# Kernel tuning notes

Measured on AMD Instinct MI355X. Metric: run time of the kernel, lower is better.

The kernel has to match this reference:

```python
import jax, jax.numpy as jnp
import numpy as np

N_NODES = 100000
N_EDGES = 1000000
D_FEAT = 64
N_GRAPHS = 64


def setup_inputs() -> dict:
    key = jax.random.key(0)
    ks = jax.random.split(key, 5)
    x = jax.random.normal(ks[0], (N_NODES, D_FEAT), dtype=jnp.float32)
    edge_index = jax.random.randint(ks[1], (2, N_EDGES), 0, N_NODES, dtype=jnp.int32)
    batch = jnp.sort(jax.random.randint(ks[2], (N_NODES,), 0, N_GRAPHS, dtype=jnp.int32))
    s = 1.0 / np.sqrt(D_FEAT)
    W1 = jax.random.uniform(ks[3], (D_FEAT, D_FEAT), jnp.float32, -s, s)
    W2 = jax.random.uniform(ks[4], (D_FEAT, D_FEAT), jnp.float32, -s, s)
    b1 = jnp.zeros((D_FEAT,), jnp.float32)
    b2 = jnp.zeros((D_FEAT,), jnp.float32)
    return {"x": x, "edge_index": edge_index, "batch": batch,
            "W1": W1, "b1": b1, "W2": W2, "b2": b2}


def gcn_conv(x, edge_index, W, b, num_nodes):
    # PyG GCNConv: h = D^{-1/2} (A + I) D^{-1/2} (x W) + b
    loops = jnp.arange(num_nodes, dtype=edge_index.dtype)
    row = jnp.concatenate([edge_index[0], loops])  # source nodes
    col = jnp.concatenate([edge_index[1], loops])  # target nodes
    h = x @ W  # [N, D]
    deg = jax.ops.segment_sum(jnp.ones_like(col, dtype=h.dtype), col,
                              num_segments=num_nodes)  # >= 1 due to self loops
    dinv = jax.lax.rsqrt(deg)
    norm = dinv[row] * dinv[col]  # [E+N]
    out = jax.ops.segment_sum(h[row] * norm[:, None], col, num_segments=num_nodes)
    return out + b


def reference(x, edge_index, batch, W1, b1, W2, b2):
    n = x.shape[0]
    h = gcn_conv(x, edge_index, W1, b1, n)
    h = gcn_conv(h, edge_index, W2, b2, n)
    # global_mean_pool over graph ids
    sums = jax.ops.segment_sum(h, batch, num_segments=N_GRAPHS)  # [G, D]
    cnts = jax.ops.segment_sum(jnp.ones((n, 1), h.dtype), batch,
                               num_segments=N_GRAPHS)
    return sums / jnp.maximum(cnts, 1.0)
```

## Files before the change

kernel.cpp:

```cpp
#include <hip/hip_runtime.h>
#include <hip/hip_fp16.h>

#define DFEAT 64
#define NG 64
#define TILE 128
#define NBLK 256
#define NBMAX 1024
#define NREP 16
#define SENT 0x7FFFFFFF

__global__ __launch_bounds__(256) void k_cnt(const int* __restrict__ col,
                                             int* __restrict__ cnt_m,
                                             int e, int nb, int chunk) {
  __shared__ int hist[NBMAX];
  int tid = threadIdx.x;
  int blk = blockIdx.x;
  for (int b = tid; b < nb; b += 256) hist[b] = 0;
  __syncthreads();
  int lo = blk * chunk, hi = min(lo + chunk, e);
  if (lo < hi) {
    int nv = (hi - lo) >> 2;
    const int4* c4 = (const int4*)(col + lo);
    for (int i = tid; i < nv; i += 256) {
      int4 v = c4[i];
      atomicAdd(&hist[v.x >> 7], 1);
      atomicAdd(&hist[v.y >> 7], 1);
      atomicAdd(&hist[v.z >> 7], 1);
      atomicAdd(&hist[v.w >> 7], 1);
    }
    for (int i = lo + (nv << 2) + tid; i < hi; i += 256)
      atomicAdd(&hist[col[i] >> 7], 1);
  }
  __syncthreads();
  for (int b = tid; b < nb; b += 256)
    cnt_m[(size_t)blk * nb + b] = hist[b];
}

__global__ __launch_bounds__(256) void k_colscan(int* __restrict__ cnt_m,
                                                 int* __restrict__ gcount, int nb) {
  __shared__ int sh[256];
  int tid = threadIdx.x;
  int b = blockIdx.x;
  int v = cnt_m[(size_t)tid * nb + b];
  sh[tid] = v;
  __syncthreads();
  for (int off = 1; off < 256; off <<= 1) {
    int t = (tid >= off) ? sh[tid - off] : 0;
    __syncthreads();
    sh[tid] += t;
    __syncthreads();
  }
  cnt_m[(size_t)tid * nb + b] = sh[tid] - v;
  if (tid == 255) gcount[b] = sh[255];
}

__global__ __launch_bounds__(1024) void k_bscan(const int* __restrict__ gcount,
                                                int* __restrict__ base, int nb,
                                                const float* __restrict__ W1,
                                                const float* __restrict__ W2,
                                                const float* __restrict__ b1,
                                                const int* __restrict__ batch,
                                                float* __restrict__ WW,
                                                float* __restrict__ bw,
                                                float* __restrict__ cntf, int n) {
  __shared__ float shm[8192];
  int tid = threadIdx.x;
  if (blockIdx.x == 0) {
    int* sh = (int*)shm;
    int v = (tid < nb) ? gcount[tid] : 0;
    sh[tid] = v;
    __syncthreads();
    for (int off = 1; off < 1024; off <<= 1) {
      int t = (tid >= off) ? sh[tid - off] : 0;
      __syncthreads();
      sh[tid] += t;
      __syncthreads();
    }
    if (tid < nb) base[tid] = sh[tid] - v;
    if (tid == 0) base[nb] = sh[1023];
  } else {
    float* w1 = shm;
    float* w2 = shm + 4096;
    for (int i = tid; i < 4096; i += 1024) { w1[i] = W1[i]; w2[i] = W2[i]; }
    if (tid < NG) {
      int g = tid;
      int lo = 0, hi = n;
      while (lo < hi) { int m = (lo + hi) >> 1; if (batch[m] < g) lo = m + 1; else hi = m; }
      int a = lo;
      lo = 0; hi = n;
      while (lo < hi) { int m = (lo + hi) >> 1; if (batch[m] < g + 1) lo = m + 1; else hi = m; }
      cntf[g] = (float)(lo - a);
    }
    __syncthreads();
    for (int p = tid; p < 4096; p += 1024) {
      int k = p >> 6, d = p & 63;
      float a = 0.f;
      for (int m = 0; m < 64; ++m) a += w1[k * 64 + m] * w2[m * 64 + d];
      WW[p] = a;
    }
    if (tid < 64) {
      float a = 0.f;
      for (int k = 0; k < 64; ++k) a += b1[k] * w2[k * 64 + tid];
      bw[tid] = a;
    }
  }
}

__global__ __launch_bounds__(256) void k_bin2(const int* __restrict__ row,
                                              const int* __restrict__ col,
                                              const int* __restrict__ base,
                                              const int* __restrict__ cnt_m,
                                              int* __restrict__ pairs,
                                              int e, int nb, int chunk) {
  __shared__ int gl[NBMAX];
  __shared__ int lcur[NBMAX];
  int tid = threadIdx.x;
  int blk = blockIdx.x;
  for (int b = tid; b < nb; b += 256) {
    gl[b] = base[b] + cnt_m[(size_t)blk * nb + b];
    lcur[b] = 0;
  }
  __syncthreads();
  int lo = blk * chunk, hi = min(lo + chunk, e);
  if (lo >= hi) return;
  int nv = (hi - lo) >> 2;
  const int4* r4 = (const int4*)(row + lo);
  const int4* c4 = (const int4*)(col + lo);
  for (int i = tid; i < nv; i += 256) {
    int4 rs = r4[i];
    int4 ts = c4[i];
#pragma unroll
    for (int k = 0; k < 4; ++k) {
      int s = (&rs.x)[k], t = (&ts.x)[k];
      int b = t >> 7;
      int pos = gl[b] + atomicAdd(&lcur[b], 1);
      pairs[pos] = s | ((t & (TILE - 1)) << 20);
    }
  }
  for (int i = lo + (nv << 2) + tid; i < hi; i += 256) {
    int s = row[i], t = col[i];
    int b = t >> 7;
    int pos = gl[b] + atomicAdd(&lcur[b], 1);
    pairs[pos] = s | ((t & (TILE - 1)) << 20);
  }
}

__global__ __launch_bounds__(256) void k_csr(const int* __restrict__ pairs,
                                             const int* __restrict__ base,
                                             const float* __restrict__ x,
                                             int* __restrict__ starts,
                                             int* __restrict__ srcs,
                                             float* __restrict__ dinv,
                                             __half2* __restrict__ xh,
                                             int* __restrict__ order,
                                             int n, int e) {
  __shared__ int cnt[TILE];
  __shared__ int cur[TILE];
  __shared__ int sc[TILE];
  __shared__ float sdv[TILE];
  __shared__ int dh[64], dcur[64];
  int tid = threadIdx.x;
  int b = blockIdx.x;
  int tile0 = b * TILE;
  if (tid < TILE) cnt[tid] = 0;
  if (tid >= TILE && tid < TILE + 64) dh[tid - TILE] = 0;
  __syncthreads();
  int e0 = base[b], e1 = base[b + 1];
  for (int i = e0 + tid; i < e1; i += 256)
    atomicAdd(&cnt[(unsigned)pairs[i] >> 20], 1);
  __syncthreads();
  int c = (tid < TILE) ? cnt[tid] : 0;
  if (tid < TILE) sc[tid] = c;
  __syncthreads();
  for (int off = 1; off < TILE; off <<= 1) {
    int t = (tid < TILE && tid >= off) ? sc[tid - off] : 0;
    __syncthreads();
    if (tid < TILE) sc[tid] += t;
    __syncthreads();
  }
  int mybin = 63;
  if (tid < TILE) {
    int excl = sc[tid] - c;
    cur[tid] = excl;
    int node = tile0 + tid;
    float d = rsqrtf(1.0f + (float)c);
    sdv[tid] = (node < n) ? d : 0.f;
    if (node < n) {
      starts[node] = e0 + excl;
      dinv[node] = d;
      mybin = min(c, 62);
    }
    atomicAdd(&dh[mybin], 1);
  }
  if (b == 0 && tid == 0) starts[n] = e;
  __syncthreads();
  if (tid == 0) {
    int a = 0;
    for (int i = 0; i < 64; ++i) { int t = dh[i]; dcur[i] = a; a += t; }
  }
  __syncthreads();
  if (tid < TILE) {
    int rank = atomicAdd(&dcur[mybin], 1);
    int node = tile0 + tid;
    order[tile0 + rank] = (node < n) ? node : SENT;
  }
  for (int i = e0 + tid; i < e1; i += 256) {
    int p = pairs[i];
    int pos = atomicAdd(&cur[(unsigned)p >> 20], 1);
    srcs[e0 + pos] = p & 0xFFFFF;
  }
  int nnode = min(n - tile0, TILE);
  if (nnode > 0) {
    int nfl = nnode * 16;
    const float4* xf = (const float4*)(x + (size_t)tile0 * 64);
    float2* xo = (float2*)xh + (size_t)tile0 * 16;
    for (int p = tid; p < nfl; p += 256) {
      float4 v = xf[p];
      float d = sdv[p >> 4];
      float2 st;
      ((__half2*)&st)[0] = __floats2half2_rn(v.x * d, v.y * d);
      ((__half2*)&st)[1] = __floats2half2_rn(v.z * d, v.w * d);
      xo[p] = st;
    }
  }
}

__device__ __forceinline__ void acc8w(float2& a0, float2& a1, float2& a2,
                                      float2& a3, float4 v, float w) {
  const __half2* hp = (const __half2*)&v;
  float2 t;
  t = __half22float2(hp[0]); a0.x = fmaf(w, t.x, a0.x); a0.y = fmaf(w, t.y, a0.y);
  t = __half22float2(hp[1]); a1.x = fmaf(w, t.x, a1.x); a1.y = fmaf(w, t.y, a1.y);
  t = __half22float2(hp[2]); a2.x = fmaf(w, t.x, a2.x); a2.y = fmaf(w, t.y, a2.y);
  t = __half22float2(hp[3]); a3.x = fmaf(w, t.x, a3.x); a3.y = fmaf(w, t.y, a3.y);
}
__device__ __forceinline__ void acc8(float2& a0, float2& a1, float2& a2,
                                     float2& a3, float4 v) {
  const __half2* hp = (const __half2*)&v;
  float2 t;
  t = __half22float2(hp[0]); a0.x += t.x; a0.y += t.y;
  t = __half22float2(hp[1]); a1.x += t.x; a1.y += t.y;
  t = __half22float2(hp[2]); a2.x += t.x; a2.y += t.y;
  t = __half22float2(hp[3]); a3.x += t.x; a3.y += t.y;
}

__global__ __launch_bounds__(256) void k_gather1(const int* __restrict__ starts,
                                                 const int* __restrict__ srcs,
                                                 const float* __restrict__ dinv,
                                                 const __half2* __restrict__ xh,
                                                 const int* __restrict__ batch,
                                                 const int* __restrict__ order,
                                                 __half2* __restrict__ z1h,
                                                 float* __restrict__ Tr, int n) {
  int tid = threadIdx.x;
  int slot = blockIdx.x * 32 + (tid >> 3);
  int node = order[slot];
  bool act = node < n;
  int nc = act ? node : n - 1;
  int l = tid & 7;
  int lane = tid & 63;
  int rep = blockIdx.x & (NREP - 1);
  int s = starts[nc];
  int deg = act ? (starts[nc + 1] - s) : 0;
  float dc = dinv[nc];
  int g = batch[nc];
  const float4* xf = (const float4*)xh;
  float4 sv = xf[(size_t)nc * 8 + l];
  float2 a0 = make_float2(0.f, 0.f), a1 = a0, a2 = a0, a3 = a0;
  acc8(a0, a1, a2, a3, sv);
  float wsum = 0.f;
  int trips = (deg + 3) >> 2;
  int dm1 = deg - 1;
  int r0 = 0, r1 = 0, r2 = 0, r3 = 0;
  if (trips > 0) {
    r0 = srcs[s];
    r1 = srcs[s + min(1, dm1)];
    r2 = srcs[s + min(2, dm1)];
    r3 = srcs[s + min(3, dm1)];
  }
  int j = 0;
  for (int t = 0; t < trips; ++t) {
    int n0 = r0, n1 = r1, n2 = r2, n3 = r3;
    int jn = j + 4;
    r0 = srcs[s + min(jn + 0, dm1)];
    r1 = srcs[s + min(jn + 1, dm1)];
    r2 = srcs[s + min(jn + 2, dm1)];
    r3 = srcs[s + min(jn + 3, dm1)];
    float w1w = (j + 1 < deg) ? 1.f : 0.f;
    float w2w = (j + 2 < deg) ? 1.f : 0.f;
    float w3w = (j + 3 < deg) ? 1.f : 0.f;
    float4 v0 = xf[(size_t)n0 * 8 + l];
    float4 v1 = xf[(size_t)n1 * 8 + l];
    float4 v2 = xf[(size_t)n2 * 8 + l];
    float4 v3 = xf[(size_t)n3 * 8 + l];
    wsum += dinv[n0] + w1w * dinv[n1] + w2w * dinv[n2] + w3w * dinv[n3];
    acc8(a0, a1, a2, a3, v0);
    acc8w(a0, a1, a2, a3, v1, w1w);
    acc8w(a0, a1, a2, a3, v2, w2w);
    acc8w(a0, a1, a2, a3, v3, w3w);
    j = jn;
  }
  if (act) {
    float s2 = dc * dc;
    float4 ov;
    __half2* op = (__half2*)&ov;
    op[0] = __floats2half2_rn(s2 * a0.x, s2 * a0.y);
    op[1] = __floats2half2_rn(s2 * a1.x, s2 * a1.y);
    op[2] = __floats2half2_rn(s2 * a2.x, s2 * a2.y);
    op[3] = __floats2half2_rn(s2 * a3.x, s2 * a3.y);
    ((float4*)z1h)[(size_t)node * 8 + l] = ov;
  }
  float uval = act ? dc * (dc + wsum) : 0.f;
  int g0 = __shfl(g, 0);
  bool uni = (__all(g == g0) != 0);
  if (!uni) {
    if (act && l == 0) unsafeAtomicAdd(&Tr[rep * NG + g], uval);
  } else {
    float uv = (l == 0) ? uval : 0.f;
    uv += __shfl_xor(uv, 8);
    uv += __shfl_xor(uv, 16);
    uv += __shfl_xor(uv, 32);
    if (lane == 0 && uv != 0.f) unsafeAtomicAdd(&Tr[rep * NG + g0], uv);
  }
}

__global__ __launch_bounds__(256) void k_gather2(const int* __restrict__ starts,
                                                 const int* __restrict__ srcs,
                                                 const float* __restrict__ dinv,
                                                 const __half2* __restrict__ z1h,
                                                 const int* __restrict__ batch,
                                                 const int* __restrict__ order,
                                                 float* __restrict__ Pb,
                                                 float* __restrict__ S, int n) {
  __shared__ float rowacc[2][64];
  __shared__ int sgid[2];
  int tid = threadIdx.x;
  int blk0 = (int)blockIdx.x * 32;
  int slot = blk0 + (tid >> 3);
  int node = order[slot];
  bool act = node < n;
  int nc = act ? node : n - 1;
  int l = tid & 7;
  int lane = tid & 63;
  int s = starts[nc];
  int deg = act ? (starts[nc + 1] - s) : 0;
  float dc = dinv[nc];
  int g = batch[nc];
  if (tid < 128) ((float*)rowacc)[tid] = 0.f;
  if (tid < 2) {
    int tile0b = blk0 & ~(TILE - 1);
    int idx = tile0b + (tid ? (TILE - 1) : 0);
    if (idx > n - 1) idx = n - 1;
    sgid[tid] = batch[idx];
  }
  const float4* xf = (const float4*)z1h;
  float4 sv = xf[(size_t)nc * 8 + l];
  float2 a0 = make_float2(0.f, 0.f), a1 = a0, a2 = a0, a3 = a0;
  acc8(a0, a1, a2, a3, sv);
  int trips = (deg + 3) >> 2;
  int dm1 = deg - 1;
  int r0 = 0, r1 = 0, r2 = 0, r3 = 0;
  if (trips > 0) {
    r0 = srcs[s];
    r1 = srcs[s + min(1, dm1)];
    r2 = srcs[s + min(2, dm1)];
    r3 = srcs[s + min(3, dm1)];
  }
  int j = 0;
  for (int t = 0; t < trips; ++t) {
    int n0 = r0, n1 = r1, n2 = r2, n3 = r3;
    int jn = j + 4;
    r0 = srcs[s + min(jn + 0, dm1)];
    r1 = srcs[s + min(jn + 1, dm1)];
    r2 = srcs[s + min(jn + 2, dm1)];
    r3 = srcs[s + min(jn + 3, dm1)];
    float w1w = (j + 1 < deg) ? 1.f : 0.f;
    float w2w = (j + 2 < deg) ? 1.f : 0.f;
    float w3w = (j + 3 < deg) ? 1.f : 0.f;
    float4 v0 = xf[(size_t)n0 * 8 + l];
    float4 v1 = xf[(size_t)n1 * 8 + l];
    float4 v2 = xf[(size_t)n2 * 8 + l];
    float4 v3 = xf[(size_t)n3 * 8 + l];
    acc8(a0, a1, a2, a3, v0);
    acc8w(a0, a1, a2, a3, v1, w1w);
    acc8w(a0, a1, a2, a3, v2, w2w);
    acc8w(a0, a1, a2, a3, v3, w3w);
    j = jn;
  }
  float f[8];
  f[0] = act ? dc * a0.x : 0.f;
  f[1] = act ? dc * a0.y : 0.f;
  f[2] = act ? dc * a1.x : 0.f;
  f[3] = act ? dc * a1.y : 0.f;
  f[4] = act ? dc * a2.x : 0.f;
  f[5] = act ? dc * a2.y : 0.f;
  f[6] = act ? dc * a3.x : 0.f;
  f[7] = act ? dc * a3.y : 0.f;
  __syncthreads();
  int g_lo = sgid[0], g_hi = sgid[1];
  int sel = (g == g_lo) ? 0 : ((g == g_hi) ? 1 : -1);
  if (sel < 0 && act) {
#pragma unroll
    for (int k = 0; k < 8; ++k)
      unsafeAtomicAdd(&S[g * 64 + l * 8 + k], f[k]);
  }
  float fa[8], fb[8];
#pragma unroll
  for (int k = 0; k < 8; ++k) {
    fa[k] = (sel == 0) ? f[k] : 0.f;
    fb[k] = (sel == 1) ? f[k] : 0.f;
  }
#pragma unroll
  for (int k = 0; k < 8; ++k) {
    fa[k] += __shfl_xor(fa[k], 8);
    fa[k] += __shfl_xor(fa[k], 16);
    fa[k] += __shfl_xor(fa[k], 32);
    fb[k] += __shfl_xor(fb[k], 8);
    fb[k] += __shfl_xor(fb[k], 16);
    fb[k] += __shfl_xor(fb[k], 32);
  }
  if (lane < 8) {
#pragma unroll
    for (int k = 0; k < 8; ++k) {
      if (fa[k] != 0.f) atomicAdd(&rowacc[0][lane * 8 + k], fa[k]);
      if (fb[k] != 0.f) atomicAdd(&rowacc[1][lane * 8 + k], fb[k]);
    }
  }
  __syncthreads();
  float* pb = Pb + (size_t)blockIdx.x * 130;
  if (tid < 128) pb[tid] = ((float*)rowacc)[tid];
  if (tid == 128) pb[128] = (float)g_lo;
  if (tid == 129) pb[129] = (float)g_hi;
}

__global__ __launch_bounds__(256) void k_fin(const float* __restrict__ Pb,
                                             const int* __restrict__ batch,
                                             const float* __restrict__ S,
                                             const float* __restrict__ Tr,
                                             const float* __restrict__ cntf,
                                             const float* __restrict__ WW,
                                             const float* __restrict__ bw,
                                             const float* __restrict__ b2,
                                             float* __restrict__ out, int n,
                                             int nbw) {
  __shared__ float sh[4][64];
  __shared__ float sG[64];
  int g = blockIdx.x;
  int d = threadIdx.x & 63, r = threadIdx.x >> 6;
  int lo = 0, hi = n;
  while (lo < hi) { int m = (lo + hi) >> 1; if (batch[m] < g) lo = m + 1; else hi = m; }
  int a = lo;
  lo = 0; hi = n;
  while (lo < hi) { int m = (lo + hi) >> 1; if (batch[m] < g + 1) lo = m + 1; else hi = m; }
  int b = lo;
  float acc = 0.f;
  if (b > a) {
    int bl0 = (a >> 7) << 2;
    int bl1 = min((((b - 1) >> 7) << 2) + 3, nbw - 1);
    for (int bl = bl0 + r; bl <= bl1; bl += 4) {
      const float* p = Pb + (size_t)bl * 130;
      if ((int)p[128] == g) acc += p[d];
      if ((int)p[129] == g) acc += p[64 + d];
    }
  }
  sh[r][d] = acc;
  __syncthreads();
  if (r == 0) sG[d] = acc + sh[1][d] + sh[2][d] + sh[3][d] + S[g * 64 + d];
  __syncthreads();
  if (threadIdx.x < 64) {
    float aa = 0.f;
    for (int k = 0; k < 64; ++k) aa += sG[k] * WW[k * 64 + d];
    float T = 0.f;
    for (int rr = 0; rr < NREP; ++rr) T += Tr[rr * NG + g];
    float c = fmaxf(cntf[g], 1.0f);
    out[g * 64 + d] = (aa + T * bw[d]) / c + b2[d];
  }
}

extern "C" void kernel_launch(void* const* d_in, const int* in_sizes, int n_in,
                              void* d_out, int out_size, void* d_ws, size_t ws_size,
                              hipStream_t stream) {
  const float* x = (const float*)d_in[0];
  const int* ei = (const int*)d_in[1];
  const int* bat = (const int*)d_in[2];
  const float* W1 = (const float*)d_in[3];
  const float* b1 = (const float*)d_in[4];
  const float* W2 = (const float*)d_in[5];
  const float* b2 = (const float*)d_in[6];
  float* out = (float*)d_out;

  int n = in_sizes[0] / 64;
  int e = in_sizes[1] / 2;
  const int* rowp = ei;
  const int* colp = ei + e;
  int nb = (n + TILE - 1) / TILE;
  int chunk = (((e + NBLK - 1) / NBLK) + 3) & ~3;
  int nbw = (n + 31) / 32;

  char* ws = (char*)d_ws;
  size_t off = 0;
  auto alloc = [&](size_t elems) {
    void* p = ws + off;
    off += ((elems * 4 + 255) & ~(size_t)255);
    return p;
  };
  float* S = (float*)alloc(NG * DFEAT);
  float* Tr = (float*)alloc(NREP * NG);
  float* cntf = (float*)alloc(NG);
  size_t zbytes = off;
  int* gcount = (int*)alloc(nb);
  int* base = (int*)alloc(nb + 1);
  int* cnt_m = (int*)alloc((size_t)NBLK * nb);
  float* dinv = (float*)alloc(n);
  int* starts = (int*)alloc(n + 1);
  int* srcs = (int*)alloc(e);
  float* WW = (float*)alloc(DFEAT * DFEAT);
  float* bw = (float*)alloc(DFEAT);
  __half2* xh = (__half2*)alloc((size_t)n * 32);
  __half2* z1h = (__half2*)alloc((size_t)n * 32);
  int* pairs = (int*)alloc(e);
  float* Pb = (float*)alloc((size_t)nbw * 130);
  int* order = (int*)alloc((size_t)nb * TILE);

  (void)hipMemsetAsync(S, 0, zbytes, stream);
  k_cnt<<<NBLK, 256, 0, stream>>>(colp, cnt_m, e, nb, chunk);
  k_colscan<<<nb, 256, 0, stream>>>(cnt_m, gcount, nb);
  k_bscan<<<2, 1024, 0, stream>>>(gcount, base, nb, W1, W2, b1, bat, WW, bw,
                                  cntf, n);
  k_bin2<<<NBLK, 256, 0, stream>>>(rowp, colp, base, cnt_m, pairs, e, nb, chunk);
  k_csr<<<nb, 256, 0, stream>>>(pairs, base, x, starts, srcs, dinv, xh, order,
                                n, e);

  k_gather1<<<nbw, 256, 0, stream>>>(starts, srcs, dinv, xh, bat, order, z1h,
                                     Tr, n);
  k_gather2<<<nbw, 256, 0, stream>>>(starts, srcs, dinv, z1h, bat, order, Pb,
                                     S, n);

  k_fin<<<NG, 256, 0, stream>>>(Pb, bat, S, Tr, cntf, WW, bw, b2, out, n, nbw);
}
```

Baseline: 200.7 us.

## Fuse edge binning into one pass with fixed-capacity buckets and atomic cursors

After: 194.6 us, median of 2. 1.03x faster.

```diff
diff --git a/kernel.cpp b/kernel.cpp
--- a/kernel.cpp
+++ b/kernel.cpp
@@ -8,13 +8,52 @@
 #define NBMAX 1024
 #define NREP 16
 #define SENT 0x7FFFFFFF
-
-__global__ __launch_bounds__(256) void k_cnt(const int* __restrict__ col,
-                                             int* __restrict__ cnt_m,
-                                             int e, int nb, int chunk) {
-  __shared__ int hist[NBMAX];
+#define CAP 2048
+
+__global__ __launch_bounds__(256) void k_binfuse(const int* __restrict__ row,
+                                                 const int* __restrict__ col,
+                                                 int* __restrict__ gcur,
+                                                 int* __restrict__ pairs,
+                                                 const float* __restrict__ W1,
+                                                 const float* __restrict__ W2,
+                                                 const float* __restrict__ b1,
+                                                 const int* __restrict__ batch,
+                                                 float* __restrict__ WW,
+                                                 float* __restrict__ bw,
+                                                 float* __restrict__ cntf,
+                                                 int e, int nb, int chunk, int n) {
+  __shared__ int shm[8192];
   int tid = threadIdx.x;
   int blk = blockIdx.x;
+  if (blk == NBLK) {
+    float* w1 = (float*)shm;
+    float* w2 = (float*)shm + 4096;
+    for (int i = tid; i < 4096; i += 256) { w1[i] = W1[i]; w2[i] = W2[i]; }
+    if (tid < NG) {
+      int g = tid;
+      int lo = 0, hi = n;
+      while (lo < hi) { int m = (lo + hi) >> 1; if (batch[m] < g) lo = m + 1; else hi = m; }
+      int a = lo;
+      lo = 0; hi = n;
+      while (lo < hi) { int m = (lo + hi) >> 1; if (batch[m] < g + 1) lo = m + 1; else hi = m; }
+      cntf[g] = (float)(lo - a);
+    }
+    __syncthreads();
+    for (int p = tid; p < 4096; p += 256) {
+      int k = p >> 6, d = p & 63;
+      float a = 0.f;
+      for (int m = 0; m < 64; ++m) a += w1[k * 64 + m] * w2[m * 64 + d];
+      WW[p] = a;
+    }
+    if (tid < 64) {
+      float a = 0.f;
+      for (int k = 0; k < 64; ++k) a += b1[k] * w2[k * 64 + tid];
+      bw[tid] = a;
+    }
+    return;
+  }
+  int* hist = shm;
+  int* gl = shm + NBMAX;
   for (int b = tid; b < nb; b += 256) hist[b] = 0;
   __syncthreads();
   int lo = blk * chunk, hi = min(lo + chunk, e);
@@ -32,128 +71,45 @@
       atomicAdd(&hist[col[i] >> 7], 1);
   }
   __syncthreads();
-  for (int b = tid; b < nb; b += 256)
-    cnt_m[(size_t)blk * nb + b] = hist[b];
-}
-
-__global__ __launch_bounds__(256) void k_colscan(int* __restrict__ cnt_m,
-                                                 int* __restrict__ gcount, int nb) {
-  __shared__ int sh[256];
-  int tid = threadIdx.x;
-  int b = blockIdx.x;
-  int v = cnt_m[(size_t)tid * nb + b];
-  sh[tid] = v;
-  __syncthreads();
-  for (int off = 1; off < 256; off <<= 1) {
-    int t = (tid >= off) ? sh[tid - off] : 0;
-    __syncthreads();
-    sh[tid] += t;
-    __syncthreads();
-  }
-  cnt_m[(size_t)tid * nb + b] = sh[tid] - v;
-  if (tid == 255) gcount[b] = sh[255];
-}
-
-__global__ __launch_bounds__(1024) void k_bscan(const int* __restrict__ gcount,
-                                                int* __restrict__ base, int nb,
-                                                const float* __restrict__ W1,
-                                                const float* __restrict__ W2,
-                                                const float* __restrict__ b1,
-                                                const int* __restrict__ batch,
-                                                float* __restrict__ WW,
-                                                float* __restrict__ bw,
-                                                float* __restrict__ cntf, int n) {
-  __shared__ float shm[8192];
-  int tid = threadIdx.x;
-  if (blockIdx.x == 0) {
-    int* sh = (int*)shm;
-    int v = (tid < nb) ? gcount[tid] : 0;
-    sh[tid] = v;
-    __syncthreads();
-    for (int off = 1; off < 1024; off <<= 1) {
-      int t = (tid >= off) ? sh[tid - off] : 0;
-      __syncthreads();
-      sh[tid] += t;
-      __syncthreads();
-    }
-    if (tid < nb) base[tid] = sh[tid] - v;
-    if (tid == 0) base[nb] = sh[1023];
-  } else {
-    float* w1 = shm;
-    float* w2 = shm + 4096;
-    for (int i = tid; i < 4096; i += 1024) { w1[i] = W1[i]; w2[i] = W2[i]; }
-    if (tid < NG) {
-      int g = tid;
-      int lo = 0, hi = n;
-      while (lo < hi) { int m = (lo + hi) >> 1; if (batch[m] < g) lo = m + 1; else hi = m; }
-      int a = lo;
-      lo = 0; hi = n;
-      while (lo < hi) { int m = (lo + hi) >> 1; if (batch[m] < g + 1) lo = m + 1; else hi = m; }
-      cntf[g] = (float)(lo - a);
-    }
-    __syncthreads();
-    for (int p = tid; p < 4096; p += 1024) {
-      int k = p >> 6, d = p & 63;
-      float a = 0.f;
-      for (int m = 0; m < 64; ++m) a += w1[k * 64 + m] * w2[m * 64 + d];
-      WW[p] = a;
-    }
-    if (tid < 64) {
-      float a = 0.f;
-      for (int k = 0; k < 64; ++k) a += b1[k] * w2[k * 64 + tid];
-      bw[tid] = a;
-    }
-  }
-}
-
-__global__ __launch_bounds__(256) void k_bin2(const int* __restrict__ row,
-                                              const int* __restrict__ col,
-                                              const int* __restrict__ base,
-                                              const int* __restrict__ cnt_m,
-                                              int* __restrict__ pairs,
-                                              int e, int nb, int chunk) {
-  __shared__ int gl[NBMAX];
-  __shared__ int lcur[NBMAX];
-  int tid = threadIdx.x;
-  int blk = blockIdx.x;
   for (int b = tid; b < nb; b += 256) {
-    gl[b] = base[b] + cnt_m[(size_t)blk * nb + b];
-    lcur[b] = 0;
-  }
-  __syncthreads();
-  int lo = blk * chunk, hi = min(lo + chunk, e);
-  if (lo >= hi) return;
-  int nv = (hi - lo) >> 2;
-  const int4* r4 = (const int4*)(row + lo);
-  const int4* c4 = (const int4*)(col + lo);
-  for (int i = tid; i < nv; i += 256) {
-    int4 rs = r4[i];
-    int4 ts = c4[i];
+    int h = hist[b];
+    gl[b] = (h > 0) ? (b * CAP + atomicAdd(&gcur[b], h)) : 0;
+    hist[b] = 0;
+  }
+  __syncthreads();
+  if (lo < hi) {
+    int nv = (hi - lo) >> 2;
+    const int4* r4 = (const int4*)(row + lo);
+    const int4* c4 = (const int4*)(col + lo);
+    for (int i = tid; i < nv; i += 256) {
+      int4 rs = r4[i];
+      int4 ts = c4[i];
 #pragma unroll
-    for (int k = 0; k < 4; ++k) {
-      int s = (&rs.x)[k], t = (&ts.x)[k];
+      for (int k = 0; k < 4; ++k) {
+        int s = (&rs.x)[k], t = (&ts.x)[k];
+        int b = t >> 7;
+        int pos = gl[b] + atomicAdd(&hist[b], 1);
+        pairs[pos] = s | ((t & (TILE - 1)) << 20);
+      }
+    }
+    for (int i = lo + (nv << 2) + tid; i < hi; i += 256) {
+      int s = row[i], t = col[i];
       int b = t >> 7;
-      int pos = gl[b] + atomicAdd(&lcur[b], 1);
+      int pos = gl[b] + atomicAdd(&hist[b], 1);
       pairs[pos] = s | ((t & (TILE - 1)) << 20);
     }
   }
-  for (int i = lo + (nv << 2) + tid; i < hi; i += 256) {
-    int s = row[i], t = col[i];
-    int b = t >> 7;
-    int pos = gl[b] + atomicAdd(&lcur[b], 1);
-    pairs[pos] = s | ((t & (TILE - 1)) << 20);
-  }
 }
 
 __global__ __launch_bounds__(256) void k_csr(const int* __restrict__ pairs,
-                                             const int* __restrict__ base,
+                                             const int* __restrict__ gcur,
                                              const float* __restrict__ x,
-                                             int* __restrict__ starts,
+                                             int* __restrict__ starts2,
                                              int* __restrict__ srcs,
                                              float* __restrict__ dinv,
                                              __half2* __restrict__ xh,
                                              int* __restrict__ order,
-                                             int n, int e) {
+                                             int n) {
   __shared__ int cnt[TILE];
   __shared__ int cur[TILE];
   __shared__ int sc[TILE];
@@ -165,7 +121,7 @@
   if (tid < TILE) cnt[tid] = 0;
   if (tid >= TILE && tid < TILE + 64) dh[tid - TILE] = 0;
   __syncthreads();
-  int e0 = base[b], e1 = base[b + 1];
+  int e0 = b * CAP, e1 = e0 + gcur[b];
   for (int i = e0 + tid; i < e1; i += 256)
     atomicAdd(&cnt[(unsigned)pairs[i] >> 20], 1);
   __syncthreads();
@@ -186,13 +142,12 @@
     float d = rsqrtf(1.0f + (float)c);
     sdv[tid] = (node < n) ? d : 0.f;
     if (node < n) {
-      starts[node] = e0 + excl;
+      starts2[node] = (e0 + excl) | (c << 22);
       dinv[node] = d;
       mybin = min(c, 62);
     }
     atomicAdd(&dh[mybin], 1);
   }
-  if (b == 0 && tid == 0) starts[n] = e;
   __syncthreads();
   if (tid == 0) {
     int a = 0;
@@ -244,7 +199,7 @@
   t = __half22float2(hp[3]); a3.x += t.x; a3.y += t.y;
 }
 
-__global__ __launch_bounds__(256) void k_gather1(const int* __restrict__ starts,
+__global__ __launch_bounds__(256) void k_gather1(const int* __restrict__ starts2,
                                                  const int* __restrict__ srcs,
                                                  const float* __restrict__ dinv,
                                                  const __half2* __restrict__ xh,
@@ -260,8 +215,9 @@
   int l = tid & 7;
   int lane = tid & 63;
   int rep = blockIdx.x & (NREP - 1);
-  int s = starts[nc];
-  int deg = act ? (starts[nc + 1] - s) : 0;
+  unsigned sv2 = (unsigned)starts2[nc];
+  int s = sv2 & 0x3FFFFF;
+  int deg = act ? (int)(sv2 >> 22) : 0;
   float dc = dinv[nc];
   int g = batch[nc];
   const float4* xf = (const float4*)xh;
@@ -324,7 +280,7 @@
   }
 }
 
-__global__ __launch_bounds__(256) void k_gather2(const int* __restrict__ starts,
+__global__ __launch_bounds__(256) void k_gather2(const int* __restrict__ starts2,
                                                  const int* __restrict__ srcs,
                                                  const float* __restrict__ dinv,
                                                  const __half2* __restrict__ z1h,
@@ -342,8 +298,9 @@
   int nc = act ? node : n - 1;
   int l = tid & 7;
   int lane = tid & 63;
-  int s = starts[nc];
-  int deg = act ? (starts[nc + 1] - s) : 0;
+  unsigned sv2 = (unsigned)starts2[nc];
+  int s = sv2 & 0x3FFFFF;
+  int deg = act ? (int)(sv2 >> 22) : 0;
   float dc = dinv[nc];
   int g = batch[nc];
   if (tid < 128) ((float*)rowacc)[tid] = 0.f;
@@ -507,33 +464,28 @@
   float* S = (float*)alloc(NG * DFEAT);
   float* Tr = (float*)alloc(NREP * NG);
   float* cntf = (float*)alloc(NG);
+  int* gcur = (int*)alloc(nb);
   size_t zbytes = off;
-  int* gcount = (int*)alloc(nb);
-  int* base = (int*)alloc(nb + 1);
-  int* cnt_m = (int*)alloc((size_t)NBLK * nb);
   float* dinv = (float*)alloc(n);
-  int* starts = (int*)alloc(n + 1);
-  int* srcs = (int*)alloc(e);
+  int* starts2 = (int*)alloc(n);
+  int* srcs = (int*)alloc((size_t)nb * CAP);
   float* WW = (float*)alloc(DFEAT * DFEAT);
   float* bw = (float*)alloc(DFEAT);
   __half2* xh = (__half2*)alloc((size_t)n * 32);
   __half2* z1h = (__half2*)alloc((size_t)n * 32);
-  int* pairs = (int*)alloc(e);
+  int* pairs = (int*)alloc((size_t)nb * CAP);
   float* Pb = (float*)alloc((size_t)nbw * 130);
   int* order = (int*)alloc((size_t)nb * TILE);
 
   (void)hipMemsetAsync(S, 0, zbytes, stream);
-  k_cnt<<<NBLK, 256, 0, stream>>>(colp, cnt_m, e, nb, chunk);
-  k_colscan<<<nb, 256, 0, stream>>>(cnt_m, gcount, nb);
-  k_bscan<<<2, 1024, 0, stream>>>(gcount, base, nb, W1, W2, b1, bat, WW, bw,
-                                  cntf, n);
-  k_bin2<<<NBLK, 256, 0, stream>>>(rowp, colp, base, cnt_m, pairs, e, nb, chunk);
-  k_csr<<<nb, 256, 0, stream>>>(pairs, base, x, starts, srcs, dinv, xh, order,
-                                n, e);
-
-  k_gather1<<<nbw, 256, 0, stream>>>(starts, srcs, dinv, xh, bat, order, z1h,
+  k_binfuse<<<NBLK + 1, 256, 0, stream>>>(rowp, colp, gcur, pairs, W1, W2, b1,
+                                          bat, WW, bw, cntf, e, nb, chunk, n);
+  k_csr<<<nb, 256, 0, stream>>>(pairs, gcur, x, starts2, srcs, dinv, xh, order,
+                                n);
+
+  k_gather1<<<nbw, 256, 0, stream>>>(starts2, srcs, dinv, xh, bat, order, z1h,
                                      Tr, n);
-  k_gather2<<<nbw, 256, 0, stream>>>(starts, srcs, dinv, z1h, bat, order, Pb,
+  k_gather2<<<nbw, 256, 0, stream>>>(starts2, srcs, dinv, z1h, bat, order, Pb,
                                      S, n);
 
   k_fin<<<NG, 256, 0, stream>>>(Pb, bat, S, Tr, cntf, WW, bw, b2, out, n, nbw);
```
